# Kernel optimization log

Hardware: AMD Instinct MI355X
Metric: run time of the kernel (lower is better)

Reference implementation:

```python
import jax, jax.numpy as jnp
import numpy as np

# Module hyperparameters (from init_kwargs)
N, C, L = 8, 256, 8192
K = 3            # kernel_size
G = 8            # groups
GC = C // G      # group channels = 32
PAD = 1
DIL = 1
OFFSET_SCALE = 1.0
LN_EPS = 1e-6


def setup_inputs() -> dict:
    key = jax.random.key(0)
    k1, k2, k3, k4, k5 = jax.random.split(key, 5)
    x = jax.random.normal(k1, (N, C, L), dtype=jnp.float32)
    # LayerNorm affine params
    ln_w = 1.0 + 0.1 * jax.random.normal(k2, (C,), dtype=jnp.float32)
    ln_b = 0.1 * jax.random.normal(k3, (C,), dtype=jnp.float32)
    # offset/mask linear: C -> G*K*2 (zero-init in the module; small random here
    # so the deformable sampling path is exercised non-trivially)
    om_w = 0.02 * jax.random.normal(k4, (G * K * 2, C), dtype=jnp.float32)
    om_b = 0.02 * jax.random.normal(k5, (G * K * 2,), dtype=jnp.float32)
    return {"x": x, "ln_w": ln_w, "ln_b": ln_b, "om_w": om_w, "om_b": om_b}


def _dcnv4_1d(x, ln_w, ln_b, om_w, om_b):
    # x: [N, C, L]
    xt = jnp.transpose(x, (0, 2, 1))                       # [N, L, C]
    # LayerNorm over channels
    mu = xt.mean(-1, keepdims=True)
    var = xt.var(-1, keepdims=True)
    xn = (xt - mu) * jax.lax.rsqrt(var + LN_EPS) * ln_w + ln_b
    xa = jax.nn.gelu(xn, approximate=False)                # [N, L, C]

    # offset / mask projection
    om = jnp.einsum('nlc,oc->nlo', xa, om_w) + om_b        # [N, L, 2*G*K]
    off = om[..., : G * K].reshape(N, L, G, K)             # [N, L, G, K]
    mask = om[..., G * K:].reshape(N, L, G, K)             # [N, L, G, K]

    # sampling positions: conv grid + learned offsets
    base = (jnp.arange(L, dtype=jnp.float32)[:, None] - PAD
            + DIL * jnp.arange(K, dtype=jnp.float32)[None, :])   # [L, K]
    p = base[None, :, None, :] + OFFSET_SCALE * off        # [N, L, G, K]

    p0 = jnp.floor(p)
    w1 = p - p0                                            # linear interp weight
    w0 = 1.0 - w1
    i0 = p0.astype(jnp.int32)
    i1 = i0 + 1
    v0 = ((i0 >= 0) & (i0 < L)).astype(x.dtype)
    v1 = ((i1 >= 0) & (i1 < L)).astype(x.dtype)
    w0 = w0 * v0
    w1 = w1 * v1
    i0c = jnp.clip(i0, 0, L - 1)
    i1c = jnp.clip(i1, 0, L - 1)

    # group the features: [N, G, GC, L]
    xg = jnp.transpose(xa.reshape(N, L, G, GC), (0, 2, 3, 1))

    def gather(idx):  # idx: [N, L, G, K] -> values [N, G, GC, L, K]
        it = jnp.transpose(idx, (0, 2, 1, 3)).reshape(N, G, 1, L * K)
        it = jnp.broadcast_to(it, (N, G, GC, L * K))
        return jnp.take_along_axis(xg, it, axis=3).reshape(N, G, GC, L, K)

    samp = gather(i0c) * jnp.transpose(w0, (0, 2, 1, 3))[:, :, None] \
         + gather(i1c) * jnp.transpose(w1, (0, 2, 1, 3))[:, :, None]  # [N,G,GC,L,K]

    # mask-weighted aggregation over kernel taps (DCNv4: raw mask, no softmax)
    out = jnp.einsum('ngclk,nlgk->ngcl', samp, mask)       # [N, G, GC, L]
    return out.reshape(N, C, L)


def reference(x, ln_w, ln_b, om_w, om_b):
    return _dcnv4_1d(x, ln_w, ln_b, om_w, om_b)
```

## Files before the change

### kernel.cpp

```cpp
#include <hip/hip_runtime.h>
#include <hip/hip_bf16.h>
#include <math.h>

#define NN 8
#define CC 256
#define LL 8192
#define KK 3
#define GG 8
#define GCC 32
#define OMD 48
#define TL 32
#define FT 64

typedef __attribute__((ext_vector_type(8))) short short8v;
typedef __attribute__((ext_vector_type(4))) float floatx4;

__device__ inline ushort f2bf(float f) {
    uint u = __float_as_uint(f);
    u += 0x7fffu + ((u >> 16) & 1u);
    return (ushort)(u >> 16);
}

__device__ inline float gelu_fast(float xn) {
    float u = xn * xn;
    float z = xn * (-1.5957691216f - 0.0713548162726f * u);
    return __fdividef(xn, 1.f + __expf(z));
}

__global__ __launch_bounds__(256, 6) void k_ln_gelu(
    const float* __restrict__ x,
    const float* __restrict__ ln_w, const float* __restrict__ ln_b,
    __hip_bfloat16* __restrict__ xa)
{
    __shared__ __align__(16) float xs[128 * 33];
    int n  = blockIdx.y;
    int l0 = blockIdx.x * TL;
    int t  = threadIdx.x;
    int p   = t >> 3;
    int sub = t & 7;
    int pp  = p ^ (sub << 2);

    const float* xbase = x + (size_t)n * CC * LL + l0;
    float r[32];

    float4 v[8];
    #pragma unroll
    for (int it = 0; it < 8; ++it) {
        int idx = it * 256 + t;
        int c   = idx >> 3;
        int l4  = idx & 7;
        v[it] = *reinterpret_cast<const float4*>(xbase + (size_t)c * LL + l4 * 4);
    }

    #pragma unroll
    for (int half = 0; half < 2; ++half) {
        if (half) __syncthreads();
        #pragma unroll
        for (int it = 0; it < 4; ++it) {
            int idx = (half * 4 + it) * 256 + t;
            int cl  = (idx >> 3) & 127;
            int l4  = idx & 7;
            int sw  = (cl >> 4) << 2;
            int b   = cl * 33;
            float4 vv = v[half * 4 + it];
            xs[b + ((4 * l4 + 0) ^ sw)] = vv.x;
            xs[b + ((4 * l4 + 1) ^ sw)] = vv.y;
            xs[b + ((4 * l4 + 2) ^ sw)] = vv.z;
            xs[b + ((4 * l4 + 3) ^ sw)] = vv.w;
        }
        __syncthreads();
        #pragma unroll
        for (int j = 0; j < 16; ++j)
            r[half * 16 + j] = xs[(sub * 16 + j) * 33 + pp];
    }

    float sum = 0.f, sq = 0.f;
    #pragma unroll
    for (int j = 0; j < 32; ++j) { sum += r[j]; sq = fmaf(r[j], r[j], sq); }
    #pragma unroll
    for (int m = 1; m <= 4; m <<= 1) {
        sum += __shfl_xor(sum, m);
        sq  += __shfl_xor(sq, m);
    }
    float mean = sum * (1.f / 256.f);
    float rstd = rsqrtf(sq * (1.f / 256.f) - mean * mean + 1e-6f);

    __syncthreads();
    uint4* xb4 = reinterpret_cast<uint4*>(xs);

    #pragma unroll
    for (int half = 0; half < 2; ++half) {
        int cb = half * 128 + sub * 16;
        ushort pk[16];
        #pragma unroll
        for (int q = 0; q < 4; ++q) {
            float4 lw = *reinterpret_cast<const float4*>(ln_w + cb + 4 * q);
            float4 lb = *reinterpret_cast<const float4*>(ln_b + cb + 4 * q);
            float lww[4] = {lw.x, lw.y, lw.z, lw.w};
            float lbb[4] = {lb.x, lb.y, lb.z, lb.w};
            #pragma unroll
            for (int i = 0; i < 4; ++i) {
                int j = 4 * q + i;
                float xn = (r[half * 16 + j] - mean) * rstd * lww[i] + lbb[i];
                pk[j] = f2bf(gelu_fast(xn));
            }
        }
        #pragma unroll
        for (int q = 0; q < 2; ++q) {
            uint4 w4;
            w4.x = (uint)pk[8*q+0] | ((uint)pk[8*q+1] << 16);
            w4.y = (uint)pk[8*q+2] | ((uint)pk[8*q+3] << 16);
            w4.z = (uint)pk[8*q+4] | ((uint)pk[8*q+5] << 16);
            w4.w = (uint)pk[8*q+6] | ((uint)pk[8*q+7] << 16);
            xb4[p * 33 + (cb >> 3) + q] = w4;
        }
    }
    __syncthreads();

    #pragma unroll
    for (int it = 0; it < 4; ++it) {
        int idx = it * 256 + t;
        int row = idx >> 5;
        int col = idx & 31;
        uint4* dst = reinterpret_cast<uint4*>(xa + ((size_t)n * LL + l0 + row) * CC);
        dst[col] = xb4[row * 33 + col];
    }
}

__global__ __launch_bounds__(256, 4) void k_fused(
    const __hip_bfloat16* __restrict__ xa, const float* __restrict__ om_w,
    const float* __restrict__ om_b, float* __restrict__ out)
{
    __shared__ __align__(16) uint4 uPool[1536];
    __shared__ float om_s[FT * 49];

    int t  = threadIdx.x;
    int n  = blockIdx.y;
    int l0 = blockIdx.x * FT;

    ushort* wL = reinterpret_cast<ushort*>(uPool);

    #pragma unroll 12
    for (int it = 0; it < 48; ++it) {
        int idx = it * 256 + t;
        int o   = idx >> 8;
        int c   = idx & 255;
        int nt  = o >> 4;
        int ks  = c >> 5;
        int qq  = (c & 31) >> 3;
        int j   = c & 7;
        int lane = (o & 15) | (qq << 4);
        wL[((ks * 3 + nt) * 64 + lane) * 8 + j] = f2bf(om_w[idx]);
    }
    __syncthreads();

    int lane = t & 63;
    int wv   = t >> 6;
    int col  = lane & 15;
    int q    = lane >> 4;
    const ushort* xp = reinterpret_cast<const ushort*>(xa);
    const short8v* A0 = reinterpret_cast<const short8v*>(
        xp + ((size_t)n * LL + l0 + wv * 16 + col) * CC + q * 8);
    const short8v* Bb = reinterpret_cast<const short8v*>(wL) + lane;

    floatx4 c0 = {0.f,0.f,0.f,0.f}, c1 = {0.f,0.f,0.f,0.f}, c2 = {0.f,0.f,0.f,0.f};
    #pragma unroll
    for (int ks = 0; ks < 8; ++ks) {
        short8v a = A0[ks * 4];
        c0 = __builtin_amdgcn_mfma_f32_16x16x32_bf16(a, Bb[(ks*3+0)*64], c0, 0, 0, 0);
        c1 = __builtin_amdgcn_mfma_f32_16x16x32_bf16(a, Bb[(ks*3+1)*64], c1, 0, 0, 0);
        c2 = __builtin_amdgcn_mfma_f32_16x16x32_bf16(a, Bb[(ks*3+2)*64], c2, 0, 0, 0);
    }
    float b0 = om_b[col];
    float b1 = om_b[16 + col];
    float b2 = om_b[32 + col];
    #pragma unroll
    for (int i = 0; i < 4; ++i) {
        int row = wv * 16 + q * 4 + i;
        om_s[row * 49 + col]      = c0[i] + b0;
        om_s[row * 49 + 16 + col] = c1[i] + b1;
        om_s[row * 49 + 32 + col] = c2[i] + b2;
    }
    __syncthreads();

    int cq = t & 3;
    int ps = t >> 2;
    int c4 = t & 15;
    int rw = t >> 4;
    size_t xb2 = (size_t)n * LL * CC;
    float* outs = reinterpret_cast<float*>(uPool);
    float* ob0 = outs;
    float* ob1 = outs + (GCC * 68);
    int colw = ps ^ (cq << 3);

    #pragma unroll
    for (int gp = 0; gp < GG; gp += 2) {
        const __hip_bfloat16* xab0 = xa + xb2 + (size_t)(gp + 0) * GCC + cq * 8;
        const __hip_bfloat16* xab1 = xa + xb2 + (size_t)(gp + 1) * GCC + cq * 8;
        float acc0[8] = {0.f,0.f,0.f,0.f,0.f,0.f,0.f,0.f};
        float acc1[8] = {0.f,0.f,0.f,0.f,0.f,0.f,0.f,0.f};
        #pragma unroll
        for (int k = 0; k < KK; ++k) {
            float base = (float)(l0 + ps - 1 + k);
            float off0  = om_s[ps * 49 + (gp + 0) * KK + k];
            float msk0  = om_s[ps * 49 + 24 + (gp + 0) * KK + k];
            float pA  = base + off0;
            float pA0 = floorf(pA);
            float wA1 = pA - pA0;
            int iA0 = (int)pA0;
            int iA1 = iA0 + 1;
            float aA0 = (iA0 >= 0 && iA0 < LL) ? msk0 * (1.f - wA1) : 0.f;
            float aA1 = (iA1 >= 0 && iA1 < LL) ? msk0 * wA1 : 0.f;
            iA0 = min(max(iA0, 0), LL - 1);
            iA1 = min(max(iA1, 0), LL - 1);
            float off1  = om_s[ps * 49 + (gp + 1) * KK + k];
            float msk1  = om_s[ps * 49 + 24 + (gp + 1) * KK + k];
            float pB  = base + off1;
            float pB0 = floorf(pB);
            float wB1 = pB - pB0;
            int iB0 = (int)pB0;
            int iB1 = iB0 + 1;
            float aB0 = (iB0 >= 0 && iB0 < LL) ? msk1 * (1.f - wB1) : 0.f;
            float aB1 = (iB1 >= 0 && iB1 < LL) ? msk1 * wB1 : 0.f;
            iB0 = min(max(iB0, 0), LL - 1);
            iB1 = min(max(iB1, 0), LL - 1);

            uint4 rA0 = *reinterpret_cast<const uint4*>(xab0 + (size_t)iA0 * CC);
            uint4 rA1 = *reinterpret_cast<const uint4*>(xab0 + (size_t)iA1 * CC);
            uint4 rB0 = *reinterpret_cast<const uint4*>(xab1 + (size_t)iB0 * CC);
            uint4 rB1 = *reinterpret_cast<const uint4*>(xab1 + (size_t)iB1 * CC);
            uint uA0[4] = {rA0.x, rA0.y, rA0.z, rA0.w};
            uint uA1[4] = {rA1.x, rA1.y, rA1.z, rA1.w};
            uint uB0[4] = {rB0.x, rB0.y, rB0.z, rB0.w};
            uint uB1[4] = {rB1.x, rB1.y, rB1.z, rB1.w};
            #pragma unroll
            for (int d = 0; d < 4; ++d) {
                acc0[2*d]   = fmaf(aA0, __uint_as_float(uA0[d] << 16),
                              fmaf(aA1, __uint_as_float(uA1[d] << 16), acc0[2*d]));
                acc0[2*d+1] = fmaf(aA0, __uint_as_float(uA0[d] & 0xffff0000u),
                              fmaf(aA1, __uint_as_float(uA1[d] & 0xffff0000u), acc0[2*d+1]));
                acc1[2*d]   = fmaf(aB0, __uint_as_float(uB0[d] << 16),
                              fmaf(aB1, __uint_as_float(uB1[d] << 16), acc1[2*d]));
                acc1[2*d+1] = fmaf(aB0, __uint_as_float(uB0[d] & 0xffff0000u),
                              fmaf(aB1, __uint_as_float(uB1[d] & 0xffff0000u), acc1[2*d+1]));
            }
        }
        #pragma unroll
        for (int j = 0; j < 8; ++j) {
            int row = cq * 8 + j;
            ob0[row * 68 + colw] = acc0[j];
            ob1[row * 68 + colw] = acc1[j];
        }
        __syncthreads();

        float* op0 = out + ((size_t)n * CC + (size_t)(gp + 0) * GCC) * LL + l0;
        float* op1 = op0 + (size_t)GCC * LL;
        #pragma unroll
        for (int rr = 0; rr < 2; ++rr) {
            int row = rw + rr * 16;
            int colr = (c4 * 4) ^ ((row >> 3) << 3);
            float4 v0 = *reinterpret_cast<const float4*>(&ob0[row * 68 + colr]);
            float4 v1 = *reinterpret_cast<const float4*>(&ob1[row * 68 + colr]);
            *reinterpret_cast<float4*>(op0 + (size_t)row * LL + c4 * 4) = v0;
            *reinterpret_cast<float4*>(op1 + (size_t)row * LL + c4 * 4) = v1;
        }
        if (gp < GG - 2) __syncthreads();
    }
}

extern "C" void kernel_launch(void* const* d_in, const int* in_sizes, int n_in,
                              void* d_out, int out_size, void* d_ws, size_t ws_size,
                              hipStream_t stream) {
    const float* x    = (const float*)d_in[0];
    const float* ln_w = (const float*)d_in[1];
    const float* ln_b = (const float*)d_in[2];
    const float* om_w = (const float*)d_in[3];
    const float* om_b = (const float*)d_in[4];
    float* out = (float*)d_out;

    __hip_bfloat16* xa = (__hip_bfloat16*)((char*)d_ws + 49152);

    dim3 g1(LL / TL, NN);
    k_ln_gelu<<<g1, 256, 0, stream>>>(x, ln_w, ln_b, xa);

    dim3 g2(LL / FT, NN);
    k_fused<<<g2, 256, 0, stream>>>(xa, om_w, om_b, out);
}
```

Baseline: 51.27 us.

## Split fused deformable sampling kernel across two group halves via grid z

Adds a z dimension of 2 to the fused kernel grid, so each block handles four of the eight groups. Each block keeps only the offset and mask columns for its half in a smaller shared buffer. This doubles block count to raise parallelism and shorten per-block latency. In exchange, each block still loads the full projection weights and recomputes the whole projection, duplicating that work.

```diff
diff --git a/kernel.cpp b/kernel.cpp
--- a/kernel.cpp
+++ b/kernel.cpp
@@ -132,11 +132,13 @@
     const float* __restrict__ om_b, float* __restrict__ out)
 {
     __shared__ __align__(16) uint4 uPool[1536];
-    __shared__ float om_s[FT * 49];
+    __shared__ float om_s[FT * 25];
 
     int t  = threadIdx.x;
     int n  = blockIdx.y;
+    int h  = blockIdx.z;
     int l0 = blockIdx.x * FT;
+    int h12 = 12 * h;
 
     ushort* wL = reinterpret_cast<ushort*>(uPool);
 
@@ -177,9 +179,15 @@
     #pragma unroll
     for (int i = 0; i < 4; ++i) {
         int row = wv * 16 + q * 4 + i;
-        om_s[row * 49 + col]      = c0[i] + b0;
-        om_s[row * 49 + 16 + col] = c1[i] + b1;
-        om_s[row * 49 + 32 + col] = c2[i] + b2;
+        float* os = om_s + row * 25;
+        float vals[3] = {c0[i] + b0, c1[i] + b1, c2[i] + b2};
+        int   gcs[3]  = {col, 16 + col, 32 + col};
+        #pragma unroll
+        for (int f = 0; f < 3; ++f) {
+            int gc = gcs[f];
+            if (gc >= h12 && gc < h12 + 12)               os[gc - h12] = vals[f];
+            else if (gc >= 24 + h12 && gc < 36 + h12)     os[12 + gc - 24 - h12] = vals[f];
+        }
     }
     __syncthreads();
 
@@ -194,16 +202,17 @@
     int colw = ps ^ (cq << 3);
 
     #pragma unroll
-    for (int gp = 0; gp < GG; gp += 2) {
-        const __hip_bfloat16* xab0 = xa + xb2 + (size_t)(gp + 0) * GCC + cq * 8;
-        const __hip_bfloat16* xab1 = xa + xb2 + (size_t)(gp + 1) * GCC + cq * 8;
+    for (int gp = 0; gp < 4; gp += 2) {
+        int g0 = 4 * h + gp;
+        const __hip_bfloat16* xab0 = xa + xb2 + (size_t)(g0 + 0) * GCC + cq * 8;
+        const __hip_bfloat16* xab1 = xa + xb2 + (size_t)(g0 + 1) * GCC + cq * 8;
         float acc0[8] = {0.f,0.f,0.f,0.f,0.f,0.f,0.f,0.f};
         float acc1[8] = {0.f,0.f,0.f,0.f,0.f,0.f,0.f,0.f};
         #pragma unroll
         for (int k = 0; k < KK; ++k) {
             float base = (float)(l0 + ps - 1 + k);
-            float off0  = om_s[ps * 49 + (gp + 0) * KK + k];
-            float msk0  = om_s[ps * 49 + 24 + (gp + 0) * KK + k];
+            float off0  = om_s[ps * 25 + (gp + 0) * 3 + k];
+            float msk0  = om_s[ps * 25 + 12 + (gp + 0) * 3 + k];
             float pA  = base + off0;
             float pA0 = floorf(pA);
             float wA1 = pA - pA0;
@@ -213,8 +222,8 @@
             float aA1 = (iA1 >= 0 && iA1 < LL) ? msk0 * wA1 : 0.f;
             iA0 = min(max(iA0, 0), LL - 1);
             iA1 = min(max(iA1, 0), LL - 1);
-            float off1  = om_s[ps * 49 + (gp + 1) * KK + k];
-            float msk1  = om_s[ps * 49 + 24 + (gp + 1) * KK + k];
+            float off1  = om_s[ps * 25 + (gp + 1) * 3 + k];
+            float msk1  = om_s[ps * 25 + 12 + (gp + 1) * 3 + k];
             float pB  = base + off1;
             float pB0 = floorf(pB);
             float wB1 = pB - pB0;
@@ -253,7 +262,7 @@
         }
         __syncthreads();
 
-        float* op0 = out + ((size_t)n * CC + (size_t)(gp + 0) * GCC) * LL + l0;
+        float* op0 = out + ((size_t)n * CC + (size_t)(g0 + 0) * GCC) * LL + l0;
         float* op1 = op0 + (size_t)GCC * LL;
         #pragma unroll
         for (int rr = 0; rr < 2; ++rr) {
@@ -264,7 +273,7 @@
             *reinterpret_cast<float4*>(op0 + (size_t)row * LL + c4 * 4) = v0;
             *reinterpret_cast<float4*>(op1 + (size_t)row * LL + c4 * 4) = v1;
         }
-        if (gp < GG - 2) __syncthreads();
+        if (gp == 0) __syncthreads();
     }
 }
 
@@ -283,6 +292,6 @@
     dim3 g1(LL / TL, NN);
     k_ln_gelu<<<g1, 256, 0, stream>>>(x, ln_w, ln_b, xa);
 
-    dim3 g2(LL / FT, NN);
+    dim3 g2(LL / FT, NN, 2);
     k_fused<<<g2, 256, 0, stream>>>(xa, om_w, om_b, out);
 }
```

Result: slower. 57.45 us (+12.0%).
